# Kernel tuning notes

Measured on AMD Instinct MI355X. Metric: run time of the kernel, lower is better.

Reference implementation:

```python
import jax, jax.numpy as jnp
import numpy as np

B, L, D = 16, 2048, 128
NEG = -1.0e9


def setup_inputs() -> dict:
    key = jax.random.key(0)
    kq, kk, kv, km = jax.random.split(key, 4)
    Q = jax.random.normal(kq, (B, L, D), dtype=jnp.float32)
    K = jax.random.normal(kk, (B, L, D), dtype=jnp.float32)
    V = jax.random.normal(kv, (B, L, D), dtype=jnp.float32)
    scale = jnp.float32(1.0 / np.sqrt(D))
    # original code masks rows where (mask + 1) == 0, i.e. mask == -1
    mask = jnp.where(jax.random.uniform(km, (B, L)) < 0.1, -1, 0).astype(jnp.int32)
    return {"Q": Q, "K": K, "V": V, "scale": scale, "mask": mask}


def reference(Q, K, V, scale, mask):
    # attention = Q @ K^T * scale  -> [B, Lq, Lk]
    att = jnp.einsum("bqd,bkd->bqk", Q, K) * scale
    # mask[b, i] broadcast over the key dim j (row-wise masking, as in the
    # original unsqueeze(-1).expand pattern with square attention)
    row_masked = (mask + 1) == 0  # [B, L]
    att = jnp.where(row_masked[:, :, None], NEG, att)
    att = jax.nn.softmax(att, axis=-1)
    context = jnp.einsum("bqk,bkd->bqd", att, V)
    return context
```

## Files before the change

### kernel.cpp

```cpp
#include <hip/hip_runtime.h>


#define NB 16
#define LL 2048
#define DD 128
#define LOG2E 1.44269504f
#define NM (-9.0f * 1.44269504f)

typedef __attribute__((ext_vector_type(8))) short short8;
typedef __attribute__((ext_vector_type(16))) float f32x16;

__device__ __forceinline__ float wexp2(float x) {
  float r; asm("v_exp_f32 %0, %1" : "=v"(r) : "v"(x)); return r;
}
__device__ __forceinline__ unsigned cvtpk(float lo, float hi) {
  unsigned r; asm("v_cvt_pk_bf16_f32 %0, %1, %2" : "=v"(r) : "v"(lo), "v"(hi)); return r;
}
__device__ __forceinline__ void gll16(const void* g, const void* l) {
  __builtin_amdgcn_global_load_lds(
      (const __attribute__((address_space(1))) unsigned*)g,
      (__attribute__((address_space(3))) unsigned*)l, 16, 0, 0);
}

__global__ void prep_qk(const float* __restrict__ Q, const float* __restrict__ K,
                        const float* __restrict__ scale, const int* __restrict__ mask,
                        short* __restrict__ Qb, short* __restrict__ Kb) {
  int bid = blockIdx.x;
  int g = ((bid & 2047) << 8) + threadIdx.x;
  if (bid < 2048) {
    float sc = scale[0];
    float msc = (mask[g >> 4] == -1) ? 0.f : sc;
    const float4* qp = (const float4*)Q + (size_t)g * 2;
    float4 a = qp[0], c = qp[1];
    ((uint4*)Qb)[g] = make_uint4(cvtpk(a.x * msc, a.y * msc), cvtpk(a.z * msc, a.w * msc),
                                 cvtpk(c.x * msc, c.y * msc), cvtpk(c.z * msc, c.w * msc));
  } else {
    const float4* kp = (const float4*)K + (size_t)g * 2;
    float4 a = kp[0], c = kp[1];
    ((uint4*)Kb)[g] = make_uint4(cvtpk(a.x, a.y), cvtpk(a.z, a.w),
                                 cvtpk(c.x, c.y), cvtpk(c.z, c.w));
  }
}

__global__ void prep_vt(const float* __restrict__ V, short* __restrict__ Vt) {
  __shared__ short lds[64 * 130];
  int b = blockIdx.x >> 5;
  int t0 = (blockIdx.x & 31) * 64;
  int t = threadIdx.x;
  #pragma unroll
  for (int i = 0; i < 8; ++i) {
    int c = t + i * 256;
    int kv = c >> 5, ds = (c & 31) * 4;
    float4 v = *(const float4*)(V + ((size_t)(b * LL + t0 + kv) * DD + ds));
    unsigned* dst = (unsigned*)(&lds[kv * 130 + ds]);
    dst[0] = cvtpk(v.x, v.y);
    dst[1] = cvtpk(v.z, v.w);
  }
  __syncthreads();
  int d = t >> 1, hf = t & 1;
  unsigned dw[16];
  #pragma unroll
  for (int i = 0; i < 16; ++i) {
    int kv = hf * 32 + i * 2;
    unsigned lo16 = (unsigned short)lds[kv * 130 + d];
    unsigned hi16 = (unsigned short)lds[(kv + 1) * 130 + d];
    dw[i] = lo16 | (hi16 << 16);
  }
  short* orow = Vt + (size_t)(b * DD + d) * LL + t0 + hf * 32;
  #pragma unroll
  for (int i = 0; i < 4; ++i)
    ((uint4*)orow)[i] = make_uint4(dw[4 * i], dw[4 * i + 1], dw[4 * i + 2], dw[4 * i + 3]);
}

__global__ __launch_bounds__(512, 2) void attn_main(
    const short* __restrict__ Qb, const short* __restrict__ Kb,
    const short* __restrict__ Vt, float* __restrict__ Out) {
  __shared__ __align__(16) char smem[99840];
  const int tid = threadIdx.x;
  const int w = tid >> 6, l = tid & 63, lo = l & 31, hi = l >> 5;
  const int qg = w & 3, kvh = w >> 2;

  int lg = (blockIdx.x & 7) * 32 + (blockIdx.x >> 3);
  int b = lg >> 4;
  int q0 = (lg & 15) * 128 + qg * 32;

  short8 qf[8];
  const short* qp = Qb + (size_t)(b * LL + q0 + lo) * DD;
  #pragma unroll
  for (int dc = 0; dc < 8; ++dc)
    qf[dc] = *(const short8*)(qp + dc * 16 + hi * 8);

  const char* kgb = (const char*)(Kb + (size_t)b * (LL * DD));
  const char* vgb = (const char*)(Vt + (size_t)b * (LL * DD));

#define STAGE(bi_, kv0_) do { \
    char* kbuf = smem + (bi_) * 16384; \
    char* vbuf = smem + 49152 + (bi_) * 16384; \
    _Pragma("unroll") \
    for (int i = 0; i < 2; ++i) { \
      int c = w * 2 + i; \
      int kr = c * 4 + (l >> 4); \
      int kc = ((l & 15) << 4) ^ ((kr & 15) << 4); \
      gll16(kgb + (size_t)((kv0_) + kr) * 256 + kc, kbuf + c * 1024); \
      int vr = c * 8 + (l >> 3); \
      int vc = ((l & 7) << 4) ^ ((vr & 7) << 4); \
      gll16(vgb + (size_t)vr * 4096 + (size_t)(kv0_) * 2 + vc, vbuf + c * 1024); \
    } \
  } while (0)

  STAGE(0, 0);
  STAGE(1, 64);

  f32x16 oacc[4];
  #pragma unroll
  for (int dt = 0; dt < 4; ++dt)
    #pragma unroll
    for (int r = 0; r < 16; ++r) oacc[dt][r] = 0.f;
  float lsum = 0.f;

  const int swzk = (lo & 15) << 4;
  const int swzv = (lo & 7) << 4;

  int cb = 0, sb = 2;
  #pragma unroll 1
  for (int t = 0; t < 32; ++t) {
    if (t == 31) { asm volatile("s_waitcnt vmcnt(0)" ::: "memory"); }
    else         { asm volatile("s_waitcnt vmcnt(4)" ::: "memory"); }
    __builtin_amdgcn_s_barrier();
    __builtin_amdgcn_sched_barrier(0);
    if (t < 30) STAGE(sb, (t + 2) * 64);

    const char* kb = smem + cb * 16384;
    const char* vb = smem + 49152 + cb * 16384;

    f32x16 acc;
    #pragma unroll
    for (int r = 0; r < 16; ++r) acc[r] = 0.f;
    const char* krow = kb + (kvh * 32 + lo) * 256;
    #pragma unroll
    for (int dc = 0; dc < 8; ++dc) {
      short8 kf = *(const short8*)(krow + ((dc * 32 + hi * 16) ^ swzk));
      acc = __builtin_amdgcn_mfma_f32_32x32x16_bf16(kf, qf[dc], acc, 0, 0, 0);
    }
    float ps = 0.f;
    #pragma unroll
    for (int r = 0; r < 16; ++r) {
      float p = wexp2(__builtin_fmaf(acc[r], LOG2E, NM));
      acc[r] = p; ps += p;
    }
    lsum += ps;
    short8 pa[2];
    #pragma unroll
    for (int ks = 0; ks < 2; ++ks) {
      unsigned a0 = cvtpk(acc[ks * 8 + 0], acc[ks * 8 + 1]);
      unsigned b0 = cvtpk(acc[ks * 8 + 4], acc[ks * 8 + 5]);
      unsigned c0 = cvtpk(acc[ks * 8 + 2], acc[ks * 8 + 3]);
      unsigned d0 = cvtpk(acc[ks * 8 + 6], acc[ks * 8 + 7]);
      asm volatile("v_permlane32_swap_b32 %0, %1" : "+v"(a0), "+v"(b0));
      asm volatile("v_permlane32_swap_b32 %0, %1" : "+v"(c0), "+v"(d0));
      union { unsigned u[4]; short8 s; } pu;
      pu.u[0] = a0; pu.u[1] = c0; pu.u[2] = b0; pu.u[3] = d0;
      pa[ks] = pu.s;
    }
    #pragma unroll
    for (int dt = 0; dt < 4; ++dt) {
      const char* vrow = vb + (dt * 32 + lo) * 128;
      #pragma unroll
      for (int ks = 0; ks < 2; ++ks) {
        short8 vf = *(const short8*)(vrow + ((kvh * 64 + ks * 32 + hi * 16) ^ swzv));
        oacc[dt] = __builtin_amdgcn_mfma_f32_32x32x16_bf16(pa[ks], vf, oacc[dt], 0, 0, 0);
      }
    }
    cb = (cb == 2) ? 0 : cb + 1;
    sb = (sb == 2) ? 0 : sb + 1;
  }
#undef STAGE

  float* lsb = (float*)(smem + 98304);
  float* rdb = (float*)(smem + 98304 + 1024);
  __syncthreads();
  if (kvh == 1) {
    char* reg = smem + qg * 16384;
    #pragma unroll
    for (int dt = 0; dt < 4; ++dt)
      #pragma unroll
      for (int i = 0; i < 4; ++i)
        *(float4*)(reg + l * 256 + ((dt * 64 + i * 16) ^ ((l & 15) << 4))) =
            make_float4(oacc[dt][4 * i], oacc[dt][4 * i + 1],
                        oacc[dt][4 * i + 2], oacc[dt][4 * i + 3]);
    lsb[qg * 64 + l] = lsum;
  }
  __syncthreads();
  if (kvh == 0) {
    char* reg = smem + qg * 16384;
    lsum += lsb[qg * 64 + l];
    #pragma unroll
    for (int dt = 0; dt < 4; ++dt)
      #pragma unroll
      for (int i = 0; i < 4; ++i) {
        float4 p = *(const float4*)(reg + l * 256 + ((dt * 64 + i * 16) ^ ((l & 15) << 4)));
        oacc[dt][4 * i + 0] += p.x;
        oacc[dt][4 * i + 1] += p.y;
        oacc[dt][4 * i + 2] += p.z;
        oacc[dt][4 * i + 3] += p.w;
      }
    float lt = lsum + __shfl_xor(lsum, 32);
    float rd = 1.0f / lt;
    if (l < 32) rdb[qg * 32 + l] = rd;
    #pragma unroll
    for (int r = 0; r < 16; ++r) {
      int cr = (r & 3) + 8 * (r >> 2) + 4 * hi;
      float rr = rdb[qg * 32 + cr];
      float* op = Out + (size_t)(b * LL + q0 + cr) * DD + lo;
      #pragma unroll
      for (int dt = 0; dt < 4; ++dt)
        op[dt * 32] = oacc[dt][r] * rr;
    }
  }
}

extern "C" void kernel_launch(void* const* d_in, const int* in_sizes, int n_in,
                              void* d_out, int out_size, void* d_ws, size_t ws_size,
                              hipStream_t stream) {
  const float* Q = (const float*)d_in[0];
  const float* K = (const float*)d_in[1];
  const float* V = (const float*)d_in[2];
  const float* scale = (const float*)d_in[3];
  const int* mask = (const int*)d_in[4];
  float* out = (float*)d_out;

  const size_t tensor_elems = (size_t)NB * LL * DD;
  const size_t need = 3 * tensor_elems * sizeof(short);
  if (ws_size < need) return;

  short* Qb = (short*)d_ws;
  short* Kb = Qb + tensor_elems;
  short* Vtp = Kb + tensor_elems;

  hipLaunchKernelGGL(prep_qk, dim3(4096), dim3(256), 0, stream, Q, K, scale, mask, Qb, Kb);
  hipLaunchKernelGGL(prep_vt, dim3(512), dim3(256), 0, stream, V, Vtp);
  hipLaunchKernelGGL(attn_main, dim3(256), dim3(512), 0, stream, Qb, Kb, Vtp, out);
}
```

Before: 62.62 us.

## Load K fragments directly to registers in MFMA layout, drop K LDS staging

The K prep kernel now writes bf16 K pre-permuted into the per-lane MFMA fragment order, so the attention kernel loads K fragments straight from global memory into double-buffered registers instead of staging them through LDS. V staging moves to a 4-deep LDS ring with a new swizzle, and the barrier and wait placement is restructured, with the loop unrolled by two to alternate the K register buffers. This removes LDS traffic and space for K and shrinks shared memory, at the cost of more VGPRs for the two K fragment sets and global-load latency exposed to the register path.

After: 64.52 us. +3.0%, slower.

```diff
diff --git a/kernel.cpp b/kernel.cpp
--- a/kernel.cpp
+++ b/kernel.cpp
@@ -22,9 +22,9 @@
       (__attribute__((address_space(3))) unsigned*)l, 16, 0, 0);
 }
 
-__global__ void prep_qk(const float* __restrict__ Q, const float* __restrict__ K,
-                        const float* __restrict__ scale, const int* __restrict__ mask,
-                        short* __restrict__ Qb, short* __restrict__ Kb) {
+__global__ void prep_qkf(const float* __restrict__ Q, const float* __restrict__ K,
+                         const float* __restrict__ scale, const int* __restrict__ mask,
+                         short* __restrict__ Qb, short* __restrict__ Kf) {
   int bid = blockIdx.x;
   int g = ((bid & 2047) << 8) + threadIdx.x;
   if (bid < 2048) {
@@ -35,9 +35,16 @@
     ((uint4*)Qb)[g] = make_uint4(cvtpk(a.x * msc, a.y * msc), cvtpk(a.z * msc, a.w * msc),
                                  cvtpk(c.x * msc, c.y * msc), cvtpk(c.z * msc, c.w * msc));
   } else {
-    const float4* kp = (const float4*)K + (size_t)g * 2;
+    int bt = g >> 10;
+    int rem = g & 1023;
+    int kvh = rem >> 9, rem2 = rem & 511;
+    int dc = rem2 >> 6, lf = rem2 & 63;
+    int hif = lf >> 5, lof = lf & 31;
+    int row = (bt >> 5) * LL + (bt & 31) * 64 + kvh * 32 + lof;
+    int col = dc * 16 + hif * 8;
+    const float4* kp = (const float4*)(K + (size_t)row * DD + col);
     float4 a = kp[0], c = kp[1];
-    ((uint4*)Kb)[g] = make_uint4(cvtpk(a.x, a.y), cvtpk(a.z, a.w),
+    ((uint4*)Kf)[g] = make_uint4(cvtpk(a.x, a.y), cvtpk(a.z, a.w),
                                  cvtpk(c.x, c.y), cvtpk(c.z, c.w));
   }
 }
@@ -73,9 +80,9 @@
 }
 
 __global__ __launch_bounds__(512, 2) void attn_main(
-    const short* __restrict__ Qb, const short* __restrict__ Kb,
+    const short* __restrict__ Qb, const short* __restrict__ Kf,
     const short* __restrict__ Vt, float* __restrict__ Out) {
-  __shared__ __align__(16) char smem[99840];
+  __shared__ __align__(16) char smem[67072];
   const int tid = threadIdx.x;
   const int w = tid >> 6, l = tid & 63, lo = l & 31, hi = l >> 5;
   const int qg = w & 3, kvh = w >> 2;
@@ -90,94 +97,99 @@
   for (int dc = 0; dc < 8; ++dc)
     qf[dc] = *(const short8*)(qp + dc * 16 + hi * 8);
 
-  const char* kgb = (const char*)(Kb + (size_t)b * (LL * DD));
+  const short* kfb = Kf + (size_t)b * (LL * DD) + kvh * 4096 + l * 8;
   const char* vgb = (const char*)(Vt + (size_t)b * (LL * DD));
 
-#define STAGE(bi_, kv0_) do { \
-    char* kbuf = smem + (bi_) * 16384; \
-    char* vbuf = smem + 49152 + (bi_) * 16384; \
-    _Pragma("unroll") \
-    for (int i = 0; i < 2; ++i) { \
-      int c = w * 2 + i; \
-      int kr = c * 4 + (l >> 4); \
-      int kc = ((l & 15) << 4) ^ ((kr & 15) << 4); \
-      gll16(kgb + (size_t)((kv0_) + kr) * 256 + kc, kbuf + c * 1024); \
-      int vr = c * 8 + (l >> 3); \
-      int vc = ((l & 7) << 4) ^ ((vr & 7) << 4); \
-      gll16(vgb + (size_t)vr * 4096 + (size_t)(kv0_) * 2 + vc, vbuf + c * 1024); \
+  size_t voff0, voff1;
+  {
+    int c0 = tid, c1 = tid + 512;
+    int r0 = c0 >> 5, col0 = ((c0 & 31) << 4) ^ ((r0 & 31) << 4);
+    int r1 = c1 >> 5, col1 = ((c1 & 31) << 4) ^ ((r1 & 31) << 4);
+    voff0 = (size_t)(r0 * 4 + (col0 >> 7)) * 4096 + (col0 & 127);
+    voff1 = (size_t)(r1 * 4 + (col1 >> 7)) * 4096 + (col1 & 127);
+  }
+
+#define VSTAGE(bi_, kv0_) do { \
+    char* vb_ = smem + (bi_) * 16384; \
+    gll16(vgb + voff0 + (size_t)(kv0_) * 2, vb_ + tid * 16); \
+    gll16(vgb + voff1 + (size_t)(kv0_) * 2, vb_ + tid * 16 + 8192); \
+  } while (0)
+
+#define KFLOAD(dst_, t_) do { \
+    const short* kp_ = kfb + (size_t)(t_) * 8192; \
+    _Pragma("unroll") \
+    for (int dc = 0; dc < 8; ++dc) dst_[dc] = *(const short8*)(kp_ + dc * 512); \
+  } while (0)
+
+  short8 kfA[8], kfB[8];
+  VSTAGE(0, 0);
+  VSTAGE(1, 64);
+  KFLOAD(kfA, 0);
+
+  f32x16 oacc[4];
+  #pragma unroll
+  for (int dt = 0; dt < 4; ++dt)
+    #pragma unroll
+    for (int r = 0; r < 16; ++r) oacc[dt][r] = 0.f;
+  float lsum = 0.f;
+
+#define BODY(t_, kcur_, knxt_) do { \
+    if ((t_) < 30) VSTAGE(((t_) + 2) & 3, ((t_) + 2) * 64); \
+    if ((t_) < 31) KFLOAD(knxt_, (t_) + 1); \
+    asm volatile("s_waitcnt vmcnt(10)" ::: "memory"); \
+    __builtin_amdgcn_s_barrier(); \
+    __builtin_amdgcn_sched_barrier(0); \
+    const char* vb = smem + ((t_) & 3) * 16384; \
+    f32x16 acc; \
+    _Pragma("unroll") \
+    for (int r = 0; r < 16; ++r) acc[r] = 0.f; \
+    _Pragma("unroll") \
+    for (int dc = 0; dc < 8; ++dc) \
+      acc = __builtin_amdgcn_mfma_f32_32x32x16_bf16(kcur_[dc], qf[dc], acc, 0, 0, 0); \
+    float ps = 0.f; \
+    _Pragma("unroll") \
+    for (int r = 0; r < 16; ++r) { \
+      float p = wexp2(__builtin_fmaf(acc[r], LOG2E, NM)); \
+      acc[r] = p; ps += p; \
+    } \
+    lsum += ps; \
+    short8 pa[2]; \
+    _Pragma("unroll") \
+    for (int ks = 0; ks < 2; ++ks) { \
+      unsigned a0 = cvtpk(acc[ks * 8 + 0], acc[ks * 8 + 1]); \
+      unsigned b0 = cvtpk(acc[ks * 8 + 4], acc[ks * 8 + 5]); \
+      unsigned c0 = cvtpk(acc[ks * 8 + 2], acc[ks * 8 + 3]); \
+      unsigned d0 = cvtpk(acc[ks * 8 + 6], acc[ks * 8 + 7]); \
+      asm volatile("v_permlane32_swap_b32 %0, %1" : "+v"(a0), "+v"(b0)); \
+      asm volatile("v_permlane32_swap_b32 %0, %1" : "+v"(c0), "+v"(d0)); \
+      union { unsigned u[4]; short8 s; } pu; \
+      pu.u[0] = a0; pu.u[1] = c0; pu.u[2] = b0; pu.u[3] = d0; \
+      pa[ks] = pu.s; \
+    } \
+    _Pragma("unroll") \
+    for (int dt = 0; dt < 4; ++dt) { \
+      int vrow = dt * 8 + (lo >> 2); \
+      int vcb = (lo & 3) * 128 + kvh * 64; \
+      _Pragma("unroll") \
+      for (int ks = 0; ks < 2; ++ks) { \
+        int vcol = vcb + ks * 32 + hi * 16; \
+        short8 vf = *(const short8*)(vb + vrow * 512 + (vcol ^ (vrow << 4))); \
+        oacc[dt] = __builtin_amdgcn_mfma_f32_32x32x16_bf16(pa[ks], vf, oacc[dt], 0, 0, 0); \
+      } \
     } \
   } while (0)
 
-  STAGE(0, 0);
-  STAGE(1, 64);
-
-  f32x16 oacc[4];
-  #pragma unroll
-  for (int dt = 0; dt < 4; ++dt)
-    #pragma unroll
-    for (int r = 0; r < 16; ++r) oacc[dt][r] = 0.f;
-  float lsum = 0.f;
-
-  const int swzk = (lo & 15) << 4;
-  const int swzv = (lo & 7) << 4;
-
-  int cb = 0, sb = 2;
   #pragma unroll 1
-  for (int t = 0; t < 32; ++t) {
-    if (t == 31) { asm volatile("s_waitcnt vmcnt(0)" ::: "memory"); }
-    else         { asm volatile("s_waitcnt vmcnt(4)" ::: "memory"); }
-    __builtin_amdgcn_s_barrier();
-    __builtin_amdgcn_sched_barrier(0);
-    if (t < 30) STAGE(sb, (t + 2) * 64);
-
-    const char* kb = smem + cb * 16384;
-    const char* vb = smem + 49152 + cb * 16384;
-
-    f32x16 acc;
-    #pragma unroll
-    for (int r = 0; r < 16; ++r) acc[r] = 0.f;
-    const char* krow = kb + (kvh * 32 + lo) * 256;
-    #pragma unroll
-    for (int dc = 0; dc < 8; ++dc) {
-      short8 kf = *(const short8*)(krow + ((dc * 32 + hi * 16) ^ swzk));
-      acc = __builtin_amdgcn_mfma_f32_32x32x16_bf16(kf, qf[dc], acc, 0, 0, 0);
-    }
-    float ps = 0.f;
-    #pragma unroll
-    for (int r = 0; r < 16; ++r) {
-      float p = wexp2(__builtin_fmaf(acc[r], LOG2E, NM));
-      acc[r] = p; ps += p;
-    }
-    lsum += ps;
-    short8 pa[2];
-    #pragma unroll
-    for (int ks = 0; ks < 2; ++ks) {
-      unsigned a0 = cvtpk(acc[ks * 8 + 0], acc[ks * 8 + 1]);
-      unsigned b0 = cvtpk(acc[ks * 8 + 4], acc[ks * 8 + 5]);
-      unsigned c0 = cvtpk(acc[ks * 8 + 2], acc[ks * 8 + 3]);
-      unsigned d0 = cvtpk(acc[ks * 8 + 6], acc[ks * 8 + 7]);
-      asm volatile("v_permlane32_swap_b32 %0, %1" : "+v"(a0), "+v"(b0));
-      asm volatile("v_permlane32_swap_b32 %0, %1" : "+v"(c0), "+v"(d0));
-      union { unsigned u[4]; short8 s; } pu;
-      pu.u[0] = a0; pu.u[1] = c0; pu.u[2] = b0; pu.u[3] = d0;
-      pa[ks] = pu.s;
-    }
-    #pragma unroll
-    for (int dt = 0; dt < 4; ++dt) {
-      const char* vrow = vb + (dt * 32 + lo) * 128;
-      #pragma unroll
-      for (int ks = 0; ks < 2; ++ks) {
-        short8 vf = *(const short8*)(vrow + ((kvh * 64 + ks * 32 + hi * 16) ^ swzv));
-        oacc[dt] = __builtin_amdgcn_mfma_f32_32x32x16_bf16(pa[ks], vf, oacc[dt], 0, 0, 0);
-      }
-    }
-    cb = (cb == 2) ? 0 : cb + 1;
-    sb = (sb == 2) ? 0 : sb + 1;
-  }
-#undef STAGE
-
-  float* lsb = (float*)(smem + 98304);
-  float* rdb = (float*)(smem + 98304 + 1024);
+  for (int tt = 0; tt < 16; ++tt) {
+    BODY(2 * tt, kfA, kfB);
+    BODY(2 * tt + 1, kfB, kfA);
+  }
+#undef BODY
+#undef VSTAGE
+#undef KFLOAD
+
+  float* lsb = (float*)(smem + 65536);
+  float* rdb = (float*)(smem + 66560);
   __syncthreads();
   if (kvh == 1) {
     char* reg = smem + qg * 16384;
@@ -234,10 +246,10 @@
   if (ws_size < need) return;
 
   short* Qb = (short*)d_ws;
-  short* Kb = Qb + tensor_elems;
-  short* Vtp = Kb + tensor_elems;
-
-  hipLaunchKernelGGL(prep_qk, dim3(4096), dim3(256), 0, stream, Q, K, scale, mask, Qb, Kb);
+  short* Kfp = Qb + tensor_elems;
+  short* Vtp = Kfp + tensor_elems;
+
+  hipLaunchKernelGGL(prep_qkf, dim3(4096), dim3(256), 0, stream, Q, K, scale, mask, Qb, Kfp);
   hipLaunchKernelGGL(prep_vt, dim3(512), dim3(256), 0, stream, V, Vtp);
-  hipLaunchKernelGGL(attn_main, dim3(256), dim3(512), 0, stream, Qb, Kb, Vtp, out);
-}
+  hipLaunchKernelGGL(attn_main, dim3(256), dim3(512), 0, stream, Qb, Kfp, Vtp, out);
+}
```

## Fuse Q conversion into attention kernel, merge K/V prep, add MFMA priority hints

Applied to the files above, without the earlier changes.

Q is now read as fp32 directly in the attention kernel, where the mask and scale are applied and the values converted to bf16 in registers. This removes the separate Q prep pass and its bf16 round-trip through global memory. The K conversion and V transpose are merged into a single prep launch, dropping one kernel launch. s_setprio is raised around the MFMA blocks to favour matrix issue. The cost is heavier uncoalesced fp32 Q loads in the main kernel prologue, repeated by the two kv-half waves that share each Q tile.

New measurement: 60.74 us. 1.03x faster.

```diff
diff --git a/kernel.cpp b/kernel.cpp
--- a/kernel.cpp
+++ b/kernel.cpp
@@ -22,31 +22,22 @@
       (__attribute__((address_space(3))) unsigned*)l, 16, 0, 0);
 }
 
-__global__ void prep_qk(const float* __restrict__ Q, const float* __restrict__ K,
-                        const float* __restrict__ scale, const int* __restrict__ mask,
-                        short* __restrict__ Qb, short* __restrict__ Kb) {
+__global__ void prep_kv(const float* __restrict__ K, const float* __restrict__ V,
+                        short* __restrict__ Kb, short* __restrict__ Vt) {
+  __shared__ short lds[64 * 130];
   int bid = blockIdx.x;
-  int g = ((bid & 2047) << 8) + threadIdx.x;
+  int t = threadIdx.x;
   if (bid < 2048) {
-    float sc = scale[0];
-    float msc = (mask[g >> 4] == -1) ? 0.f : sc;
-    const float4* qp = (const float4*)Q + (size_t)g * 2;
-    float4 a = qp[0], c = qp[1];
-    ((uint4*)Qb)[g] = make_uint4(cvtpk(a.x * msc, a.y * msc), cvtpk(a.z * msc, a.w * msc),
-                                 cvtpk(c.x * msc, c.y * msc), cvtpk(c.z * msc, c.w * msc));
-  } else {
+    int g = bid * 256 + t;
     const float4* kp = (const float4*)K + (size_t)g * 2;
     float4 a = kp[0], c = kp[1];
     ((uint4*)Kb)[g] = make_uint4(cvtpk(a.x, a.y), cvtpk(a.z, a.w),
                                  cvtpk(c.x, c.y), cvtpk(c.z, c.w));
-  }
-}
-
-__global__ void prep_vt(const float* __restrict__ V, short* __restrict__ Vt) {
-  __shared__ short lds[64 * 130];
-  int b = blockIdx.x >> 5;
-  int t0 = (blockIdx.x & 31) * 64;
-  int t = threadIdx.x;
+    return;
+  }
+  int vb = bid - 2048;
+  int b = vb >> 5;
+  int t0 = (vb & 31) * 64;
   #pragma unroll
   for (int i = 0; i < 8; ++i) {
     int c = t + i * 256;
@@ -73,7 +64,8 @@
 }
 
 __global__ __launch_bounds__(512, 2) void attn_main(
-    const short* __restrict__ Qb, const short* __restrict__ Kb,
+    const float* __restrict__ Q, const float* __restrict__ scl,
+    const int* __restrict__ mask, const short* __restrict__ Kb,
     const short* __restrict__ Vt, float* __restrict__ Out) {
   __shared__ __align__(16) char smem[99840];
   const int tid = threadIdx.x;
@@ -84,11 +76,23 @@
   int b = lg >> 4;
   int q0 = (lg & 15) * 128 + qg * 32;
 
+  int qrow = b * LL + q0 + lo;
+  float msc = (mask[qrow] == -1) ? 0.f : scl[0];
   short8 qf[8];
-  const short* qp = Qb + (size_t)(b * LL + q0 + lo) * DD;
-  #pragma unroll
-  for (int dc = 0; dc < 8; ++dc)
-    qf[dc] = *(const short8*)(qp + dc * 16 + hi * 8);
+  {
+    const float* qp = Q + (size_t)qrow * DD + hi * 8;
+    #pragma unroll
+    for (int dc = 0; dc < 8; ++dc) {
+      float4 a = *(const float4*)(qp + dc * 16);
+      float4 c = *(const float4*)(qp + dc * 16 + 4);
+      union { unsigned u[4]; short8 s; } pu;
+      pu.u[0] = cvtpk(a.x * msc, a.y * msc);
+      pu.u[1] = cvtpk(a.z * msc, a.w * msc);
+      pu.u[2] = cvtpk(c.x * msc, c.y * msc);
+      pu.u[3] = cvtpk(c.z * msc, c.w * msc);
+      qf[dc] = pu.s;
+    }
+  }
 
   const char* kgb = (const char*)(Kb + (size_t)b * (LL * DD));
   const char* vgb = (const char*)(Vt + (size_t)b * (LL * DD));
@@ -137,11 +141,13 @@
     #pragma unroll
     for (int r = 0; r < 16; ++r) acc[r] = 0.f;
     const char* krow = kb + (kvh * 32 + lo) * 256;
+    __builtin_amdgcn_s_setprio(1);
     #pragma unroll
     for (int dc = 0; dc < 8; ++dc) {
       short8 kf = *(const short8*)(krow + ((dc * 32 + hi * 16) ^ swzk));
       acc = __builtin_amdgcn_mfma_f32_32x32x16_bf16(kf, qf[dc], acc, 0, 0, 0);
     }
+    __builtin_amdgcn_s_setprio(0);
     float ps = 0.f;
     #pragma unroll
     for (int r = 0; r < 16; ++r) {
@@ -162,6 +168,7 @@
       pu.u[0] = a0; pu.u[1] = c0; pu.u[2] = b0; pu.u[3] = d0;
       pa[ks] = pu.s;
     }
+    __builtin_amdgcn_s_setprio(1);
     #pragma unroll
     for (int dt = 0; dt < 4; ++dt) {
       const char* vrow = vb + (dt * 32 + lo) * 128;
@@ -171,6 +178,7 @@
         oacc[dt] = __builtin_amdgcn_mfma_f32_32x32x16_bf16(pa[ks], vf, oacc[dt], 0, 0, 0);
       }
     }
+    __builtin_amdgcn_s_setprio(0);
     cb = (cb == 2) ? 0 : cb + 1;
     sb = (sb == 2) ? 0 : sb + 1;
   }
@@ -230,14 +238,12 @@
   float* out = (float*)d_out;
 
   const size_t tensor_elems = (size_t)NB * LL * DD;
-  const size_t need = 3 * tensor_elems * sizeof(short);
+  const size_t need = 2 * tensor_elems * sizeof(short);
   if (ws_size < need) return;
 
-  short* Qb = (short*)d_ws;
-  short* Kb = Qb + tensor_elems;
-  short* Vtp = Kb + tensor_elems;
-
-  hipLaunchKernelGGL(prep_qk, dim3(4096), dim3(256), 0, stream, Q, K, scale, mask, Qb, Kb);
-  hipLaunchKernelGGL(prep_vt, dim3(512), dim3(256), 0, stream, V, Vtp);
-  hipLaunchKernelGGL(attn_main, dim3(256), dim3(512), 0, stream, Qb, Kb, Vtp, out);
-}
+  short* Kbp = (short*)d_ws;
+  short* Vtp = Kbp + tensor_elems;
+
+  hipLaunchKernelGGL(prep_kv, dim3(2560), dim3(256), 0, stream, K, V, Kbp, Vtp);
+  hipLaunchKernelGGL(attn_main, dim3(256), dim3(512), 0, stream, Q, scale, mask, Kbp, Vtp, out);
+}
```
